# Kernel optimization log

Measured on AMD Instinct MI355X. Metric: run time of the kernel, lower is better.

Reference implementation:

```python
import jax, jax.numpy as jnp
import numpy as np

INF = 100000000.0
TOPK = 27


def _box_iou(a, b):
    # a: [N,4] (x1,y1,x2,y2), b: [G,4] -> iou [N,G]
    area_a = (a[:, 2] - a[:, 0]) * (a[:, 3] - a[:, 1])
    area_b = (b[:, 2] - b[:, 0]) * (b[:, 3] - b[:, 1])
    lt = jnp.maximum(a[:, None, :2], b[None, :, :2])
    rb = jnp.minimum(a[:, None, 2:], b[None, :, 2:])
    wh = jnp.clip(rb - lt, 0.0)
    inter = wh[..., 0] * wh[..., 1]
    union = area_a[:, None] + area_b[None, :] - inter
    return inter / union, union


def _assign_one(anchors, gts, tokens):
    # anchors [N,4], gts [G,4], tokens [G,T]
    N = anchors.shape[0]
    G = gts.shape[0]
    ious, _ = _box_iou(anchors, gts)  # [N,G]

    a_cx = (anchors[:, 2] + anchors[:, 0]) * 0.5
    a_cy = (anchors[:, 3] + anchors[:, 1]) * 0.5
    g_cx = (gts[:, 2] + gts[:, 0]) * 0.5
    g_cy = (gts[:, 3] + gts[:, 1]) * 0.5

    # pairwise center distance [N,G]
    dist = jnp.sqrt((a_cx[:, None] - g_cx[None, :]) ** 2 +
                    (a_cy[:, None] - g_cy[None, :]) ** 2)

    # topk nearest anchors per gt (smallest distance) -> idxs [G,TOPK]
    _, topk_idxs = jax.lax.top_k(-dist.T, TOPK)

    # candidate ious [G,TOPK]
    cand = jnp.take_along_axis(ious.T, topk_idxs, axis=1)
    iou_mean = cand.mean(axis=1)
    iou_std = cand.std(axis=1, ddof=1)  # torch.std is unbiased
    is_pos = cand >= (iou_mean + iou_std)[:, None]

    # center-inside-gt check [G,TOPK]
    ax = a_cx[topk_idxs]
    ay = a_cy[topk_idxs]
    l = ax - gts[:, 0:1]
    t = ay - gts[:, 1:2]
    r = gts[:, 2:3] - ax
    b = gts[:, 3:4] - ay
    is_in_gts = jnp.minimum(jnp.minimum(l, t), jnp.minimum(r, b)) > 0.01
    is_pos = is_pos & is_in_gts

    # scatter candidate ious into flat [G*N] buffer of -INF (indices are unique)
    flat_idx = (jnp.arange(G)[:, None] * N + topk_idxs).reshape(-1)
    vals = ious.T.reshape(-1)[flat_idx]
    scat = jnp.where(is_pos.reshape(-1), vals, -INF)
    ious_inf = jnp.full((G * N,), -INF, dtype=ious.dtype).at[flat_idx].set(scat)
    ious_inf = ious_inf.reshape(G, N).T  # [N,G]

    anchors_to_gt_values = ious_inf.max(axis=1)          # [N]
    anchors_to_gt_indexs = ious_inf.argmax(axis=1)       # [N]

    matched_gts = gts[anchors_to_gt_indexs]              # [N,4]

    T = tokens.shape[1]
    unmatched = jnp.zeros((T,), tokens.dtype).at[-1].set(1.0)
    token_labels = jnp.where((anchors_to_gt_values == -INF)[:, None],
                             unmatched[None, :],
                             tokens[anchors_to_gt_indexs])  # [N,T]
    return anchors_to_gt_values, anchors_to_gt_indexs, matched_gts, token_labels


def setup_inputs() -> dict:
    key = jax.random.key(0)
    k1, k2, k3, k4, k5 = jax.random.split(key, 5)
    B, N, G, T = 8, 100000, 64, 256
    # anchors: valid x1<x2, y1<y2 boxes on a ~1024px canvas
    a_c = jax.random.uniform(k1, (B, N, 2), jnp.float32, 0.0, 1024.0)
    a_wh = jax.random.uniform(k2, (B, N, 2), jnp.float32, 8.0, 128.0)
    anchor_boxes = jnp.concatenate([a_c - a_wh / 2, a_c + a_wh / 2], axis=-1)
    g_c = jax.random.uniform(k3, (B, G, 2), jnp.float32, 0.0, 1024.0)
    g_wh = jax.random.uniform(k4, (B, G, 2), jnp.float32, 64.0, 512.0)
    gt_boxes = jnp.concatenate([g_c - g_wh / 2, g_c + g_wh / 2], axis=-1)
    token_map = jax.random.uniform(k5, (B, G, T), jnp.float32)
    return {"anchor_boxes": anchor_boxes, "gt_boxes": gt_boxes,
            "token_map": token_map}


def reference(anchor_boxes, gt_boxes, token_map):
    return jax.vmap(_assign_one)(anchor_boxes, gt_boxes, token_map)
```

## Files before the change

### kernel.cpp

```cpp
#include <hip/hip_runtime.h>
#include <cstdint>

constexpr int B = 8, N = 100000, G = 64, T = 256, TOPK = 27;
constexpr int BN = B * N;
constexpr int CAP = 2048;
#define NEG_INF_VAL (-100000000.0f)

__global__ __launch_bounds__(256) void atss_centers_kernel(
    const float* __restrict__ anchors, float2* __restrict__ ctr)
{
#pragma clang fp contract(off)
  int i = blockIdx.x * 256 + threadIdx.x;
  if (i < BN) {
    float4 ab = ((const float4*)anchors)[i];
    ctr[i] = make_float2((ab.z + ab.x) * 0.5f, (ab.w + ab.y) * 0.5f);
  }
}

__global__ __launch_bounds__(256) void atss_assign_kernel(
    const float* __restrict__ anchors,
    const float2* __restrict__ ctr,
    const float* __restrict__ gts,
    unsigned long long* __restrict__ best)
{
#pragma clang fp contract(off)
  __shared__ float s_d[CAP];
  __shared__ int   s_i[CAP];
  __shared__ int   s_cnt;
  __shared__ int   s_sel[TOPK];
  __shared__ float s_iou[TOPK];
  __shared__ int   s_in[TOPK];
  __shared__ float s_thresh;

  const int bg  = blockIdx.x;
  const int b   = bg / G;
  const int g   = bg % G;
  const int tid = threadIdx.x;

  const float4 gbox = ((const float4*)gts)[bg];
  const float g_cx = (gbox.z + gbox.x) * 0.5f;
  const float g_cy = (gbox.w + gbox.y) * 0.5f;

  const float4*  abase = (const float4*)(anchors + (size_t)b * N * 4);
  const float2*  cbase = ctr + (size_t)b * N;

  float thr = 24.0f;
  int M = 0;
  for (int attempt = 0; attempt < 8; ++attempt) {
    if (tid == 0) s_cnt = 0;
    __syncthreads();
    for (int n = tid; n < N; n += 256) {
      float2 c = cbase[n];
      float dx = c.x - g_cx, dy = c.y - g_cy;
      float d = __fsqrt_rn(__fmul_rn(dx, dx) + __fmul_rn(dy, dy));
      if (d < thr) {
        int p = atomicAdd(&s_cnt, 1);
        if (p < CAP) { s_d[p] = d; s_i[p] = n; }
      }
    }
    __syncthreads();
    int cnt = s_cnt;
    __syncthreads();
    if (cnt >= TOPK && cnt <= CAP) { M = cnt; break; }
    thr = (cnt < TOPK) ? thr * 4.0f : thr * 0.5f;
  }

  for (int s = tid; s < M; s += 256) {
    unsigned long long pk_s =
        ((unsigned long long)__float_as_uint(s_d[s]) << 20) |
        (unsigned long long)(unsigned)s_i[s];
    int rank = 0;
    for (int j = 0; j < M; ++j) {
      unsigned long long pk_j =
          ((unsigned long long)__float_as_uint(s_d[j]) << 20) |
          (unsigned long long)(unsigned)s_i[j];
      rank += (pk_j < pk_s) ? 1 : 0;
    }
    if (rank < TOPK) s_sel[rank] = s_i[s];
  }
  __syncthreads();

  if (tid < TOPK) {
    int a = s_sel[tid];
    float4 ab = abase[a];
    float area_a = __fmul_rn(ab.z - ab.x, ab.w - ab.y);
    float area_b = __fmul_rn(gbox.z - gbox.x, gbox.w - gbox.y);
    float ltx = fmaxf(ab.x, gbox.x), lty = fmaxf(ab.y, gbox.y);
    float rbx = fminf(ab.z, gbox.z), rby = fminf(ab.w, gbox.w);
    float w = fmaxf(rbx - ltx, 0.0f), h = fmaxf(rby - lty, 0.0f);
    float inter = __fmul_rn(w, h);
    float uni = (area_a + area_b) - inter;
    s_iou[tid] = inter / uni;
    float acx = (ab.z + ab.x) * 0.5f, acy = (ab.w + ab.y) * 0.5f;
    float l = acx - gbox.x, t = acy - gbox.y;
    float r = gbox.z - acx, bt = gbox.w - acy;
    float mn = fminf(fminf(l, t), fminf(r, bt));
    s_in[tid] = (mn > 0.01f) ? 1 : 0;
  }
  __syncthreads();

  if (tid == 0) {
    float sum = 0.0f;
    for (int k = 0; k < TOPK; ++k) sum += s_iou[k];
    float mean = sum / (float)TOPK;
    float vs = 0.0f;
    for (int k = 0; k < TOPK; ++k) {
      float d = s_iou[k] - mean;
      vs += __fmul_rn(d, d);
    }
    float sd = __fsqrt_rn(vs / (float)(TOPK - 1));
    s_thresh = mean + sd;
  }
  __syncthreads();

  if (tid < TOPK) {
    float iou = s_iou[tid];
    if (s_in[tid] && iou >= s_thresh) {
      unsigned long long pk =
          ((unsigned long long)__float_as_uint(iou) << 32) |
          (unsigned long long)(0xFFFFFFFFu - (unsigned)g);
      atomicMax(&best[(size_t)b * N + s_sel[tid]], pk);
    }
  }
}

__global__ __launch_bounds__(256) void atss_write_kernel(
    const unsigned long long* __restrict__ best,
    const float* __restrict__ gts,
    const float* __restrict__ tokens,
    float* __restrict__ out)
{
  float* __restrict__ out_val = out;
  float* __restrict__ out_idx = out + (size_t)BN;
  float* __restrict__ out_mg  = out + (size_t)2 * BN;
  float* __restrict__ out_tok = out + (size_t)6 * BN;

  __shared__ int s_row[256];

  const int tid = threadIdx.x;
  const int i0  = blockIdx.x * 256;
  const int i   = i0 + tid;

  unsigned long long p = best[i];
  const int b_ = i / N;
  int g = 0;
  float val = NEG_INF_VAL;
  if (p != 0ULL) {
    g   = (int)(0xFFFFFFFFu - (unsigned)(p & 0xFFFFFFFFULL));
    val = __uint_as_float((unsigned)(p >> 32));
  }
  const int row = b_ * G + g;
  s_row[tid] = (p != 0ULL) ? row : -1;

  out_val[i] = val;
  out_idx[i] = (float)g;
  ((float4*)out_mg)[i] = ((const float4*)gts)[row];
  __syncthreads();

  const int lane = tid & 63;
  const int sub  = tid >> 6;
  const float4* tok4 = (const float4*)tokens;
#pragma unroll 4
  for (int s = 0; s < 64; ++s) {
    int a = (s << 2) + sub;
    int r = s_row[a];
    float4 t;
    if (r >= 0) {
      t = tok4[(size_t)r * 64 + lane];
    } else {
      t = make_float4(0.0f, 0.0f, 0.0f, 0.0f);
      if (lane == 63) t.w = 1.0f;
    }
    ((float4*)(out_tok + (size_t)(i0 + a) * T))[lane] = t;
  }
}

extern "C" void kernel_launch(void* const* d_in, const int* in_sizes, int n_in,
                              void* d_out, int out_size, void* d_ws, size_t ws_size,
                              hipStream_t stream) {
  const float* anchors = (const float*)d_in[0];
  const float* gts     = (const float*)d_in[1];
  const float* tokens  = (const float*)d_in[2];
  float* out = (float*)d_out;

  unsigned long long* best = (unsigned long long*)d_ws;
  float2* ctr = (float2*)((char*)d_ws + sizeof(unsigned long long) * (size_t)BN);

  hipMemsetAsync(best, 0, sizeof(unsigned long long) * (size_t)BN, stream);
  atss_centers_kernel<<<(BN + 255) / 256, 256, 0, stream>>>(anchors, ctr);
  atss_assign_kernel<<<B * G, 256, 0, stream>>>(anchors, ctr, gts, best);
  atss_write_kernel<<<BN / 256, 256, 0, stream>>>(best, gts, tokens, out);
}
```

Before: 961.1 us.

## Fuse memset into centers kernel, widen assign scan, add nontemporal output stores

Zeroing of the best buffer moves into the centers kernel, so the separate memset launch goes away. The assign kernel now uses 1024 threads and reads two centers at a time as float4. It compares squared distances and only takes a square root for candidates, and its block index is remapped so neighbouring blocks spread across batches. The write kernel uses nontemporal stores for the large output to reduce cache pollution. Comparing squared distances against a squared threshold could flip borderline candidates relative to comparing sqrt against the threshold, though the final top-k still ranks by the sqrt distance.

```diff
diff --git a/kernel.cpp b/kernel.cpp
--- a/kernel.cpp
+++ b/kernel.cpp
@@ -6,18 +6,22 @@
 constexpr int CAP = 2048;
 #define NEG_INF_VAL (-100000000.0f)
 
+typedef float v4f __attribute__((ext_vector_type(4)));
+
 __global__ __launch_bounds__(256) void atss_centers_kernel(
-    const float* __restrict__ anchors, float2* __restrict__ ctr)
+    const float* __restrict__ anchors, float2* __restrict__ ctr,
+    unsigned long long* __restrict__ best)
 {
 #pragma clang fp contract(off)
   int i = blockIdx.x * 256 + threadIdx.x;
   if (i < BN) {
     float4 ab = ((const float4*)anchors)[i];
     ctr[i] = make_float2((ab.z + ab.x) * 0.5f, (ab.w + ab.y) * 0.5f);
-  }
-}
-
-__global__ __launch_bounds__(256) void atss_assign_kernel(
+    best[i] = 0ULL;
+  }
+}
+
+__global__ __launch_bounds__(1024) void atss_assign_kernel(
     const float* __restrict__ anchors,
     const float2* __restrict__ ctr,
     const float* __restrict__ gts,
@@ -32,7 +36,8 @@
   __shared__ int   s_in[TOPK];
   __shared__ float s_thresh;
 
-  const int bg  = blockIdx.x;
+  const int bid = blockIdx.x;
+  const int bg  = (bid & 7) * (B * G / 8) + (bid >> 3);
   const int b   = bg / G;
   const int g   = bg % G;
   const int tid = threadIdx.x;
@@ -43,29 +48,36 @@
 
   const float4*  abase = (const float4*)(anchors + (size_t)b * N * 4);
   const float2*  cbase = ctr + (size_t)b * N;
-
-  float thr = 24.0f;
+  const float4*  c4    = (const float4*)cbase;
+
+  float thr2 = 24.0f * 24.0f;
   int M = 0;
   for (int attempt = 0; attempt < 8; ++attempt) {
     if (tid == 0) s_cnt = 0;
     __syncthreads();
-    for (int n = tid; n < N; n += 256) {
-      float2 c = cbase[n];
-      float dx = c.x - g_cx, dy = c.y - g_cy;
-      float d = __fsqrt_rn(__fmul_rn(dx, dx) + __fmul_rn(dy, dy));
-      if (d < thr) {
+    for (int m = tid; m < N / 2; m += 1024) {
+      float4 c = c4[m];
+      float dx0 = c.x - g_cx, dy0 = c.y - g_cy;
+      float d20 = __fmul_rn(dx0, dx0) + __fmul_rn(dy0, dy0);
+      float dx1 = c.z - g_cx, dy1 = c.w - g_cy;
+      float d21 = __fmul_rn(dx1, dx1) + __fmul_rn(dy1, dy1);
+      if (d20 < thr2) {
         int p = atomicAdd(&s_cnt, 1);
-        if (p < CAP) { s_d[p] = d; s_i[p] = n; }
+        if (p < CAP) { s_d[p] = __fsqrt_rn(d20); s_i[p] = 2 * m; }
+      }
+      if (d21 < thr2) {
+        int p = atomicAdd(&s_cnt, 1);
+        if (p < CAP) { s_d[p] = __fsqrt_rn(d21); s_i[p] = 2 * m + 1; }
       }
     }
     __syncthreads();
     int cnt = s_cnt;
     __syncthreads();
     if (cnt >= TOPK && cnt <= CAP) { M = cnt; break; }
-    thr = (cnt < TOPK) ? thr * 4.0f : thr * 0.5f;
-  }
-
-  for (int s = tid; s < M; s += 256) {
+    thr2 = (cnt < TOPK) ? thr2 * 16.0f : thr2 * 0.25f;
+  }
+
+  for (int s = tid; s < M; s += 1024) {
     unsigned long long pk_s =
         ((unsigned long long)__float_as_uint(s_d[s]) << 20) |
         (unsigned long long)(unsigned)s_i[s];
@@ -152,26 +164,27 @@
   const int row = b_ * G + g;
   s_row[tid] = (p != 0ULL) ? row : -1;
 
-  out_val[i] = val;
-  out_idx[i] = (float)g;
-  ((float4*)out_mg)[i] = ((const float4*)gts)[row];
+  __builtin_nontemporal_store(val, out_val + i);
+  __builtin_nontemporal_store((float)g, out_idx + i);
+  v4f mg = ((const v4f*)gts)[row];
+  __builtin_nontemporal_store(mg, (v4f*)out_mg + i);
   __syncthreads();
 
   const int lane = tid & 63;
   const int sub  = tid >> 6;
-  const float4* tok4 = (const float4*)tokens;
+  const v4f* tok4 = (const v4f*)tokens;
 #pragma unroll 4
   for (int s = 0; s < 64; ++s) {
     int a = (s << 2) + sub;
     int r = s_row[a];
-    float4 t;
+    v4f t;
     if (r >= 0) {
       t = tok4[(size_t)r * 64 + lane];
     } else {
-      t = make_float4(0.0f, 0.0f, 0.0f, 0.0f);
+      t = (v4f){0.0f, 0.0f, 0.0f, 0.0f};
       if (lane == 63) t.w = 1.0f;
     }
-    ((float4*)(out_tok + (size_t)(i0 + a) * T))[lane] = t;
+    __builtin_nontemporal_store(t, (v4f*)(out_tok + (size_t)(i0 + a) * T) + lane);
   }
 }
 
@@ -186,8 +199,7 @@
   unsigned long long* best = (unsigned long long*)d_ws;
   float2* ctr = (float2*)((char*)d_ws + sizeof(unsigned long long) * (size_t)BN);
 
-  hipMemsetAsync(best, 0, sizeof(unsigned long long) * (size_t)BN, stream);
-  atss_centers_kernel<<<(BN + 255) / 256, 256, 0, stream>>>(anchors, ctr);
-  atss_assign_kernel<<<B * G, 256, 0, stream>>>(anchors, ctr, gts, best);
+  atss_centers_kernel<<<BN / 256, 256, 0, stream>>>(anchors, ctr, best);
+  atss_assign_kernel<<<B * G, 1024, 0, stream>>>(anchors, ctr, gts, best);
   atss_write_kernel<<<BN / 256, 256, 0, stream>>>(best, gts, tokens, out);
 }
```

Measured after the change: 854.4 us. 11.1% less time.
